# Kernel optimization log

Measured on AMD Instinct MI355X. Metric: run time of the kernel, lower is better.

## Reference

```python
import jax, jax.numpy as jnp
import numpy as np

B, T, C = 4, 2048, 1024
E = 8           # num_experts
H = 4 * C       # expert hidden dim


def setup_inputs() -> dict:
    key = jax.random.key(0)
    ks = jax.random.split(key, 4)
    s = 0.02
    return {
        "x":  jax.random.normal(ks[0], (B, T, C), jnp.float32),
        "Wr": jax.random.normal(ks[1], (C, E), jnp.float32) * s,
        "br": jnp.zeros((E,), jnp.float32),
        "W1": jax.random.normal(ks[2], (E, C, H), jnp.float32) * s,
        "b1": jnp.zeros((E, H), jnp.float32),
        "W2": jax.random.normal(ks[3], (E, H, C), jnp.float32) * s,
        "b2": jnp.zeros((E, C), jnp.float32),
    }


def reference(x, Wr, br, W1, b1, W2, b2):
    Bs, Ts, Cs = x.shape
    n_exp = W1.shape[0]
    xf = x.reshape(-1, Cs)                      # [N, C]
    logits = xf @ Wr + br                       # [N, E]
    gates = jax.nn.softmax(logits, axis=-1)
    probs = gates.max(axis=-1)                  # top-1 gate value [N]
    idx = gates.argmax(axis=-1)                 # expert assignment [N]

    # Masked-dense dispatch: each expert processes all tokens, mask zeroes
    # non-assigned tokens (same math as gather/MLP/scatter in the original;
    # a fused grouped-GEMM kernel would avoid the redundant FLOPs).
    out = jnp.zeros_like(xf)
    for e in range(n_exp):
        h = jax.nn.gelu(xf @ W1[e] + b1[e], approximate=False)  # [N, H]
        y = h @ W2[e] + b2[e]                                   # [N, C]
        g = jnp.where(idx == e, probs, 0.0)                     # [N]
        out = out + g[:, None] * y

    # load-balance aux loss (counts are non-differentiable, as in torch no_grad)
    counts = jnp.bincount(idx, length=n_exp).astype(jnp.float32)
    frac = counts / jnp.maximum(counts.sum(), 1.0)
    uniform = 1.0 / n_exp
    aux = jnp.mean((frac - uniform) ** 2)

    return out.reshape(Bs, Ts, Cs), aux
```

## Files before the change

kernel.cpp:

```cpp
#include <hip/hip_runtime.h>
#include <hip/hip_bf16.h>
#include <stdint.h>

#define N_TOK 8192
#define C_DIM 1024
#define E_NUM 8
#define H_DIM 4096
#define ROWS_PAD 10240
#define HBLK 32
#define MT_MAX 40

typedef __attribute__((ext_vector_type(8))) short bf16x8;
typedef __attribute__((ext_vector_type(4))) float f32x4;

static __device__ __forceinline__ unsigned short f2bf(float f) {
    union { float f; unsigned u; } v; v.f = f;
    unsigned r = (v.u + 0x7FFFu + ((v.u >> 16) & 1u)) >> 16;
    return (unsigned short)r;
}

static __device__ __forceinline__ void load_lds16(const unsigned short* g, unsigned short* l) {
    __builtin_amdgcn_global_load_lds(
        (const __attribute__((address_space(1))) unsigned int*)g,
        (__attribute__((address_space(3))) unsigned int*)l, 16, 0, 0);
}

static __device__ __forceinline__ bf16x8 rfrag(const unsigned short* hb, int r, int ks, int hi) {
    int byte = r * 128 + ks * 64 + hi * 16;
    byte ^= (r & 7) << 4;
    return *(const bf16x8*)((const char*)hb + byte);
}

#define TP_STRIDE 258
__global__ __launch_bounds__(256) void transpose_w(const float* __restrict__ in,
                                                   unsigned short* __restrict__ out,
                                                   int K, int N) {
    __shared__ unsigned short tile[64 * TP_STRIDE];
    int e  = blockIdx.z;
    int n0 = blockIdx.x * 64;
    int k0 = blockIdx.y * 256;
    int t = threadIdx.x;
    int lane = t & 63;
    int w = t >> 6;

    const float* ip = in + (size_t)e * K * N + (size_t)k0 * N + n0 + lane;
    unsigned short* lrow = &tile[lane * TP_STRIDE];
#pragma unroll 8
    for (int i = 0; i < 64; i++) {
        int k = w * 64 + i;
        lrow[k] = f2bf(ip[(size_t)k * N]);
    }
    __syncthreads();

    unsigned short* op = out + (size_t)e * N * K + (size_t)n0 * K + k0;
    for (int j = 0; j < 16; j++) {
        int n = w * 16 + j;
        const unsigned* src = (const unsigned*)&tile[n * TP_STRIDE];
        unsigned* dst = (unsigned*)&op[(size_t)n * K];
        dst[lane]      = src[lane];
        dst[lane + 64] = src[lane + 64];
    }
}

__global__ void router_kernel(const float* __restrict__ x, const float* __restrict__ Wr,
                              const float* __restrict__ br,
                              float* __restrict__ probs, int* __restrict__ eidx) {
    int n = blockIdx.x * 4 + (threadIdx.x >> 6);
    int lane = threadIdx.x & 63;
    const float* xr = x + (size_t)n * C_DIM;
    double acc[E_NUM];
#pragma unroll
    for (int e = 0; e < E_NUM; e++) acc[e] = 0.0;
    for (int i = 0; i < 16; i++) {
        int c = i * 64 + lane;
        float xv = xr[c];
        const float4* wr = (const float4*)(Wr + c * E_NUM);
        float4 w0 = wr[0], w1 = wr[1];
        acc[0] += (double)xv * w0.x; acc[1] += (double)xv * w0.y;
        acc[2] += (double)xv * w0.z; acc[3] += (double)xv * w0.w;
        acc[4] += (double)xv * w1.x; acc[5] += (double)xv * w1.y;
        acc[6] += (double)xv * w1.z; acc[7] += (double)xv * w1.w;
    }
#pragma unroll
    for (int e = 0; e < E_NUM; e++) {
#pragma unroll
        for (int o = 32; o > 0; o >>= 1) acc[e] += __shfl_xor(acc[e], o, 64);
    }
    if (lane == 0) {
        float l[E_NUM];
        for (int e = 0; e < E_NUM; e++) l[e] = (float)acc[e] + br[e];
        int arg = 0; float m = l[0];
        for (int e = 1; e < E_NUM; e++) if (l[e] > m) { m = l[e]; arg = e; }
        float s = 0.f;
        for (int e = 0; e < E_NUM; e++) s += expf(l[e] - m);
        probs[n] = 1.0f / s;
        eidx[n] = arg;
    }
}

__global__ void hist_kernel(const int* __restrict__ eidx, int* __restrict__ blk_cnt) {
    __shared__ int lh[E_NUM];
    int t = threadIdx.x, b = blockIdx.x;
    if (t < E_NUM) lh[t] = 0;
    __syncthreads();
    atomicAdd(&lh[eidx[b * 256 + t]], 1);
    __syncthreads();
    if (t < E_NUM) blk_cnt[b * E_NUM + t] = lh[t];
}

__global__ void finalize_kernel(const int* __restrict__ blk_cnt, int* __restrict__ cnt,
                                int* __restrict__ seg, int* __restrict__ blockbase,
                                float* __restrict__ aux_out) {
    int e = threadIdx.x;
    int c[HBLK];
    int tot = 0;
    if (e < E_NUM) {
#pragma unroll
        for (int b = 0; b < HBLK; b++) { c[b] = blk_cnt[b * E_NUM + e]; tot += c[b]; }
    }
    int pad = ((tot + 255) >> 8) << 8;
    int sg = 0;
#pragma unroll
    for (int j = 0; j < E_NUM; j++) {
        int pj = __shfl(pad, j, 64);
        if (j < e) sg += pj;
    }
    if (e < E_NUM) {
        cnt[e] = tot;
        seg[e] = sg;
        int run = sg;
#pragma unroll
        for (int b = 0; b < HBLK; b++) { blockbase[b * E_NUM + e] = run; run += c[b]; }
        float fr = (float)tot / (float)N_TOK - 1.0f / (float)E_NUM;
        float s = fr * fr;
#pragma unroll
        for (int o = 4; o > 0; o >>= 1) s += __shfl_xor(s, o, 64);
        if (e == 0) aux_out[0] = s / (float)E_NUM;
    }
}

__global__ void gatherpos_kernel(const float* __restrict__ probs, const int* __restrict__ eidx,
                                 const int* __restrict__ blockbase, int* __restrict__ tok_row,
                                 int* __restrict__ inv_row, float* __restrict__ rowprob) {
    __shared__ int lh[E_NUM];
    int t = threadIdx.x, b = blockIdx.x;
    if (t < E_NUM) lh[t] = 0;
    __syncthreads();
    int n = b * 256 + t;
    int e = eidx[n];
    int lrank = atomicAdd(&lh[e], 1);
    int row = blockbase[b * E_NUM + e] + lrank;
    tok_row[n] = row;
    inv_row[row] = n;
    rowprob[row] = probs[n];
}

__global__ void copy_kernel(const float* __restrict__ x, const int* __restrict__ tok_row,
                            unsigned short* __restrict__ xg) {
    int n = blockIdx.x * 4 + (threadIdx.x >> 6);
    int lane = threadIdx.x & 63;
    int row = tok_row[n];
    const float4* xr = (const float4*)(x + (size_t)n * C_DIM);
    uint2* xgr = (uint2*)(xg + (size_t)row * C_DIM);
#pragma unroll
    for (int i = 0; i < 4; i++) {
        float4 v = xr[i * 64 + lane];
        uint2 p;
        p.x = (unsigned)f2bf(v.x) | ((unsigned)f2bf(v.y) << 16);
        p.y = (unsigned)f2bf(v.z) | ((unsigned)f2bf(v.w) << 16);
        xgr[i * 64 + lane] = p;
    }
}

#define STAGE(d, ab, h, G, kt) do {                                            \
    _Pragma("unroll")                                                          \
    for (int i_ = 0; i_ < 2; i_++) {                                           \
        int idx_ = i_ * 512 + tid;                                             \
        int row_ = idx_ >> 3;                                                  \
        int us_ = (idx_ & 7) ^ (row_ & 7);                                     \
        load_lds16((G) + (size_t)((h) * 128 + row_) * KDIM + (kt) * 64 + us_ * 8, \
                   &lds[d][ab][h][(i_ * 512 + (tid & ~63)) * 8]);              \
    } } while (0)

#define PHASE(D, MH, NH, LA, LB, STAGE_STMT, WAIT_STMT) do {                   \
    if (LA) {                                                                  \
        _Pragma("unroll")                                                      \
        for (int i_ = 0; i_ < 4; i_++) {                                       \
            int r_ = wm * 64 + i_ * 16 + (lane & 15);                          \
            af[i_][0] = rfrag(&lds[D][0][MH][0], r_, 0, hi);                   \
            af[i_][1] = rfrag(&lds[D][0][MH][0], r_, 1, hi);                   \
        }                                                                      \
    }                                                                          \
    if (LB) {                                                                  \
        _Pragma("unroll")                                                      \
        for (int j_ = 0; j_ < 2; j_++) {                                       \
            int c_ = wn * 32 + j_ * 16 + (lane & 15);                          \
            bf[NH][j_][0] = rfrag(&lds[D][1][NH][0], c_, 0, hi);               \
            bf[NH][j_][1] = rfrag(&lds[D][1][NH][0], c_, 1, hi);               \
        }                                                                      \
    }                                                                          \
    STAGE_STMT;                                                                \
    __builtin_amdgcn_s_barrier();                                              \
    asm volatile("s_waitcnt lgkmcnt(0)" ::: "memory");                         \
    __builtin_amdgcn_s_setprio(1);                                             \
    _Pragma("unroll")                                                          \
    for (int i_ = 0; i_ < 4; i_++) {                                           \
        _Pragma("unroll")                                                      \
        for (int j_ = 0; j_ < 2; j_++) {                                       \
            acc[MH][i_][NH][j_] = __builtin_amdgcn_mfma_f32_16x16x32_bf16(     \
                af[i_][0], bf[NH][j_][0], acc[MH][i_][NH][j_], 0, 0, 0);       \
            acc[MH][i_][NH][j_] = __builtin_amdgcn_mfma_f32_16x16x32_bf16(     \
                af[i_][1], bf[NH][j_][1], acc[MH][i_][NH][j_], 0, 0, 0);       \
        }                                                                      \
    }                                                                          \
    __builtin_amdgcn_s_setprio(0);                                             \
    WAIT_STMT;                                                                 \
    __builtin_amdgcn_s_barrier();                                              \
} while (0)

template <int KDIM, int NDIM, int EPI>
__global__ __launch_bounds__(512) void moe_gemm(
    const unsigned short* __restrict__ Ag, const unsigned short* __restrict__ Bt,
    const float* __restrict__ bias, unsigned short* __restrict__ hg,
    float* __restrict__ out, const int* __restrict__ cnt, const int* __restrict__ seg,
    const int* __restrict__ inv_row, const float* __restrict__ rowprob) {
    int mt = blockIdx.y;
    int e;
    for (e = 0; e < E_NUM; e++) {
        int te = (cnt[e] + 255) >> 8;
        if (mt < te) break;
        mt -= te;
    }
    if (e >= E_NUM) return;
    int row0 = seg[e] + mt * 256;
    int col0 = blockIdx.x * 256;

    __shared__ unsigned short lds[2][2][2][128 * 64];

    const unsigned short* Ab = Ag + (size_t)row0 * KDIM;
    const unsigned short* Bb = Bt + (size_t)e * NDIM * KDIM + (size_t)col0 * KDIM;

    int tid = threadIdx.x;
    int lane = tid & 63;
    int wv = tid >> 6;
    int wm = wv >> 2;
    int wn = wv & 3;
    int hi = lane >> 4;

    f32x4 acc[2][4][2][2] = {};
    bf16x8 af[4][2], bf[2][2][2];

    const int NT = KDIM / 64;

    STAGE(0, 0, 0, Ab, 0);
    STAGE(0, 0, 1, Ab, 0);
    STAGE(0, 1, 0, Bb, 0);
    STAGE(0, 1, 1, Bb, 0);
    STAGE(1, 0, 0, Ab, 1);
    STAGE(1, 1, 1, Bb, 1);
    STAGE(1, 0, 1, Ab, 1);
    asm volatile("s_waitcnt vmcnt(6)" ::: "memory");
    __builtin_amdgcn_s_barrier();

    for (int t = 0; t < NT; t++) {
        int d = t & 1, dn = d ^ 1;
        bool s1 = (t + 1 < NT), s2 = (t + 2 < NT);
        PHASE(d, 0, 0, 1, 1, { if (s1) STAGE(dn, 1, 0, Bb, t + 1); }, {});
        PHASE(d, 0, 1, 0, 1, { if (s2) STAGE(d, 0, 0, Ab, t + 2); }, {});
        PHASE(d, 1, 0, 1, 0, { if (s2) STAGE(d, 1, 1, Bb, t + 2); }, {});
        PHASE(d, 1, 1, 0, 0, { if (s2) STAGE(d, 0, 1, Ab, t + 2); },
              { if (s2)      { asm volatile("s_waitcnt vmcnt(6)" ::: "memory"); }
                else if (s1) { asm volatile("s_waitcnt vmcnt(0)" ::: "memory"); } });
    }

    int cl = lane & 15, rq = (lane >> 4) << 2;
#pragma unroll
    for (int MH = 0; MH < 2; MH++)
#pragma unroll
    for (int i = 0; i < 4; i++)
#pragma unroll
    for (int NH = 0; NH < 2; NH++)
#pragma unroll
    for (int j = 0; j < 2; j++) {
        int gcol = col0 + NH * 128 + wn * 32 + j * 16 + cl;
        float b = bias[e * NDIM + gcol];
        int growb = row0 + MH * 128 + wm * 64 + i * 16 + rq;
#pragma unroll
        for (int r = 0; r < 4; r++) {
            int grow = growb + r;
            float v = acc[MH][i][NH][j][r] + b;
            if (EPI == 1) {
                v = 0.5f * v * (1.0f + erff(v * 0.70710678118654752f));
                hg[(size_t)grow * NDIM + gcol] = f2bf(v);
            } else {
                int token = inv_row[grow];
                if (token >= 0) out[(size_t)token * NDIM + gcol] = rowprob[grow] * v;
            }
        }
    }
}

extern "C" void kernel_launch(void* const* d_in, const int* in_sizes, int n_in,
                              void* d_out, int out_size, void* d_ws, size_t ws_size,
                              hipStream_t stream) {
    const float* x  = (const float*)d_in[0];
    const float* Wr = (const float*)d_in[1];
    const float* br = (const float*)d_in[2];
    const float* W1 = (const float*)d_in[3];
    const float* b1 = (const float*)d_in[4];
    const float* W2 = (const float*)d_in[5];
    const float* b2 = (const float*)d_in[6];
    float* out = (float*)d_out;

    char* ws = (char*)d_ws;
    unsigned short* W1t = (unsigned short*)ws;
    unsigned short* W2t = (unsigned short*)(ws + 67108864ull);
    unsigned short* xg  = (unsigned short*)(ws + 134217728ull);
    unsigned short* hg  = (unsigned short*)(ws + 155189248ull);
    char* small = ws + 239075328ull;
    float* probs     = (float*)small;
    int*   eidx      = (int*)(small + 32768);
    float* rowprob   = (float*)(small + 65536);
    int*   inv_row   = (int*)(small + 106496);
    int*   tok_row   = (int*)(small + 147456);
    int*   blk_cnt   = (int*)(small + 180224);
    int*   blockbase = blk_cnt + HBLK * E_NUM;
    int*   cnt       = blockbase + HBLK * E_NUM;
    int*   seg       = cnt + 8;

    hipMemsetAsync(xg, 0, (size_t)ROWS_PAD * C_DIM * 2, stream);
    hipMemsetAsync(inv_row, 0xFF, ROWS_PAD * 4, stream);

    transpose_w<<<dim3(H_DIM / 64, C_DIM / 256, E_NUM), 256, 0, stream>>>(W1, W1t, C_DIM, H_DIM);
    transpose_w<<<dim3(C_DIM / 64, H_DIM / 256, E_NUM), 256, 0, stream>>>(W2, W2t, H_DIM, C_DIM);

    router_kernel<<<N_TOK / 4, 256, 0, stream>>>(x, Wr, br, probs, eidx);
    hist_kernel<<<HBLK, 256, 0, stream>>>(eidx, blk_cnt);
    finalize_kernel<<<1, 64, 0, stream>>>(blk_cnt, cnt, seg, blockbase,
                                          out + (size_t)N_TOK * C_DIM);
    gatherpos_kernel<<<HBLK, 256, 0, stream>>>(probs, eidx, blockbase, tok_row, inv_row, rowprob);
    copy_kernel<<<N_TOK / 4, 256, 0, stream>>>(x, tok_row, xg);

    moe_gemm<C_DIM, H_DIM, 1><<<dim3(H_DIM / 256, MT_MAX), 512, 0, stream>>>(
        xg, W1t, b1, hg, nullptr, cnt, seg, inv_row, rowprob);
    moe_gemm<H_DIM, C_DIM, 2><<<dim3(C_DIM / 256, MT_MAX), 512, 0, stream>>>(
        hg, W2t, b2, nullptr, out, cnt, seg, inv_row, rowprob);
}
```

Before: 616.8 us.

## Replace direct global-to-LDS loads with register-staged double-buffered GEMM pipeline

```diff
diff --git a/kernel.cpp b/kernel.cpp
--- a/kernel.cpp
+++ b/kernel.cpp
@@ -19,16 +19,9 @@
     return (unsigned short)r;
 }
 
-static __device__ __forceinline__ void load_lds16(const unsigned short* g, unsigned short* l) {
-    __builtin_amdgcn_global_load_lds(
-        (const __attribute__((address_space(1))) unsigned int*)g,
-        (__attribute__((address_space(3))) unsigned int*)l, 16, 0, 0);
-}
-
-static __device__ __forceinline__ bf16x8 rfrag(const unsigned short* hb, int r, int ks, int hi) {
-    int byte = r * 128 + ks * 64 + hi * 16;
-    byte ^= (r & 7) << 4;
-    return *(const bf16x8*)((const char*)hb + byte);
+static __device__ __forceinline__ bf16x8 rfragn(const unsigned short* base, int r, int ks, int hi) {
+    int u = (ks * 4 + hi) ^ (r & 7);
+    return *(const bf16x8*)(base + r * 64 + u * 8);
 }
 
 #define TP_STRIDE 258
@@ -172,36 +165,37 @@
     }
 }
 
-#define STAGE(d, ab, h, G, kt) do {                                            \
-    _Pragma("unroll")                                                          \
-    for (int i_ = 0; i_ < 2; i_++) {                                           \
-        int idx_ = i_ * 512 + tid;                                             \
-        int row_ = idx_ >> 3;                                                  \
-        int us_ = (idx_ & 7) ^ (row_ & 7);                                     \
-        load_lds16((G) + (size_t)((h) * 128 + row_) * KDIM + (kt) * 64 + us_ * 8, \
-                   &lds[d][ab][h][(i_ * 512 + (tid & ~63)) * 8]);              \
+#define GLD(kt) do {                                                           \
+    _Pragma("unroll")                                                          \
+    for (int i_ = 0; i_ < 4; i_++) {                                           \
+        Areg[i_] = *(const uint4*)(Ab + (size_t)(srow + i_ * 64) * KDIM + (kt) * 64 + scol); \
+        Breg[i_] = *(const uint4*)(Bb + (size_t)(srow + i_ * 64) * KDIM + (kt) * 64 + scol); \
     } } while (0)
 
-#define PHASE(D, MH, NH, LA, LB, STAGE_STMT, WAIT_STMT) do {                   \
-    if (LA) {                                                                  \
-        _Pragma("unroll")                                                      \
-        for (int i_ = 0; i_ < 4; i_++) {                                       \
-            int r_ = wm * 64 + i_ * 16 + (lane & 15);                          \
-            af[i_][0] = rfrag(&lds[D][0][MH][0], r_, 0, hi);                   \
-            af[i_][1] = rfrag(&lds[D][0][MH][0], r_, 1, hi);                   \
-        }                                                                      \
-    }                                                                          \
-    if (LB) {                                                                  \
-        _Pragma("unroll")                                                      \
-        for (int j_ = 0; j_ < 2; j_++) {                                       \
-            int c_ = wn * 32 + j_ * 16 + (lane & 15);                          \
-            bf[NH][j_][0] = rfrag(&lds[D][1][NH][0], c_, 0, hi);               \
-            bf[NH][j_][1] = rfrag(&lds[D][1][NH][0], c_, 1, hi);               \
-        }                                                                      \
-    }                                                                          \
-    STAGE_STMT;                                                                \
-    __builtin_amdgcn_s_barrier();                                              \
-    asm volatile("s_waitcnt lgkmcnt(0)" ::: "memory");                         \
+#define DSW(D) do {                                                            \
+    _Pragma("unroll")                                                          \
+    for (int i_ = 0; i_ < 4; i_++) {                                           \
+        *(uint4*)&lds[D][(srow + i_ * 64) * 64 + sus]       = Areg[i_];        \
+        *(uint4*)&lds[D][(256 + srow + i_ * 64) * 64 + sus] = Breg[i_];        \
+    } } while (0)
+
+#define FRAG_A(SB, MH) do {                                                    \
+    _Pragma("unroll")                                                          \
+    for (int i_ = 0; i_ < 4; i_++) {                                           \
+        int r_ = (MH) * 128 + wm * 64 + i_ * 16 + (lane & 15);                 \
+        af[i_][0] = rfragn(SB, r_, 0, hi);                                     \
+        af[i_][1] = rfragn(SB, r_, 1, hi);                                     \
+    } } while (0)
+
+#define FRAG_B(SB, NH) do {                                                    \
+    _Pragma("unroll")                                                          \
+    for (int j_ = 0; j_ < 2; j_++) {                                           \
+        int r_ = 256 + (NH) * 128 + wn * 32 + j_ * 16 + (lane & 15);           \
+        bf[NH][j_][0] = rfragn(SB, r_, 0, hi);                                 \
+        bf[NH][j_][1] = rfragn(SB, r_, 1, hi);                                 \
+    } } while (0)
+
+#define MMAQ(MH, NH) do {                                                      \
     __builtin_amdgcn_s_setprio(1);                                             \
     _Pragma("unroll")                                                          \
     for (int i_ = 0; i_ < 4; i_++) {                                           \
@@ -214,12 +208,13 @@
         }                                                                      \
     }                                                                          \
     __builtin_amdgcn_s_setprio(0);                                             \
-    WAIT_STMT;                                                                 \
-    __builtin_amdgcn_s_barrier();                                              \
 } while (0)
 
+#define TILEBAR() do { asm volatile("s_waitcnt lgkmcnt(0)" ::: "memory");      \
+                       __builtin_amdgcn_s_barrier(); } while (0)
+
 template <int KDIM, int NDIM, int EPI>
-__global__ __launch_bounds__(512) void moe_gemm(
+__global__ __launch_bounds__(512, 2) void moe_gemm(
     const unsigned short* __restrict__ Ag, const unsigned short* __restrict__ Bt,
     const float* __restrict__ bias, unsigned short* __restrict__ hg,
     float* __restrict__ out, const int* __restrict__ cnt, const int* __restrict__ seg,
@@ -235,7 +230,7 @@
     int row0 = seg[e] + mt * 256;
     int col0 = blockIdx.x * 256;
 
-    __shared__ unsigned short lds[2][2][2][128 * 64];
+    __shared__ unsigned short lds[2][512 * 64];
 
     const unsigned short* Ab = Ag + (size_t)row0 * KDIM;
     const unsigned short* Bb = Bt + (size_t)e * NDIM * KDIM + (size_t)col0 * KDIM;
@@ -247,30 +242,35 @@
     int wn = wv & 3;
     int hi = lane >> 4;
 
+    int srow = tid >> 3;
+    int scol = (tid & 7) * 8;
+    int sus  = (((tid & 7) ^ (srow & 7))) * 8;
+
     f32x4 acc[2][4][2][2] = {};
     bf16x8 af[4][2], bf[2][2][2];
+    uint4 Areg[4], Breg[4];
 
     const int NT = KDIM / 64;
 
-    STAGE(0, 0, 0, Ab, 0);
-    STAGE(0, 0, 1, Ab, 0);
-    STAGE(0, 1, 0, Bb, 0);
-    STAGE(0, 1, 1, Bb, 0);
-    STAGE(1, 0, 0, Ab, 1);
-    STAGE(1, 1, 1, Bb, 1);
-    STAGE(1, 0, 1, Ab, 1);
-    asm volatile("s_waitcnt vmcnt(6)" ::: "memory");
-    __builtin_amdgcn_s_barrier();
+    GLD(0);
+    DSW(0);
+    GLD(1);
+    TILEBAR();
 
     for (int t = 0; t < NT; t++) {
         int d = t & 1, dn = d ^ 1;
-        bool s1 = (t + 1 < NT), s2 = (t + 2 < NT);
-        PHASE(d, 0, 0, 1, 1, { if (s1) STAGE(dn, 1, 0, Bb, t + 1); }, {});
-        PHASE(d, 0, 1, 0, 1, { if (s2) STAGE(d, 0, 0, Ab, t + 2); }, {});
-        PHASE(d, 1, 0, 1, 0, { if (s2) STAGE(d, 1, 1, Bb, t + 2); }, {});
-        PHASE(d, 1, 1, 0, 0, { if (s2) STAGE(d, 0, 1, Ab, t + 2); },
-              { if (s2)      { asm volatile("s_waitcnt vmcnt(6)" ::: "memory"); }
-                else if (s1) { asm volatile("s_waitcnt vmcnt(0)" ::: "memory"); } });
+        const unsigned short* sb = &lds[d][0];
+        FRAG_A(sb, 0);
+        FRAG_B(sb, 0);
+        if (t + 1 < NT) DSW(dn);
+        if (t + 2 < NT) GLD(t + 2);
+        MMAQ(0, 0);
+        FRAG_B(sb, 1);
+        MMAQ(0, 1);
+        FRAG_A(sb, 1);
+        MMAQ(1, 0);
+        MMAQ(1, 1);
+        TILEBAR();
     }
 
     int cl = lane & 15, rq = (lane >> 4) << 2;
```

Measured after the change: 1.025 ms. +66.1%, slower.
